# Kernel tuning notes

Measured on AMD Instinct MI355X. Metric: run time of the kernel, lower is better.

The kernel has to match this reference:

```python
import jax, jax.numpy as jnp
import numpy as np

P = 64      # num_proxies
S = 4096    # num_samples
D = 128     # embed_dim
H = 2       # nhead
HD = D // H # head dim


def _edge_index():
    # dense bipartite edges: (p -> s) and (s -> p) for every proxy/sample pair
    p = np.arange(P)
    s = np.arange(S) + P
    pp = np.repeat(p, S)
    ss = np.tile(s, P)
    src = np.concatenate([pp, ss])
    dst = np.concatenate([ss, pp])
    return jnp.asarray(np.stack([src, dst]), dtype=jnp.int32)  # [2, 2*P*S]


def setup_inputs() -> dict:
    key = jax.random.key(0)
    ks = jax.random.split(key, 13)
    lin = lambda k, o, i: jax.random.normal(k, (o, i), dtype=jnp.float32) * (1.0 / np.sqrt(i))
    return {
        "x": jax.random.normal(ks[0], (S, D), dtype=jnp.float32),
        "proxies": jax.random.normal(ks[1], (P, D), dtype=jnp.float32),
        "Wq": lin(ks[2], D, D), "bq": jnp.zeros((D,), jnp.float32),
        "Wk": lin(ks[3], D, D), "bk": jnp.zeros((D,), jnp.float32),
        "Wv": lin(ks[4], D, D), "bv": jnp.zeros((D,), jnp.float32),
        "Wo": lin(ks[5], D, D), "bo": jnp.zeros((D,), jnp.float32),
        "Wfc": lin(ks[6], D, D), "bfc": jnp.zeros((D,), jnp.float32),
        "edge_index": _edge_index(),
    }


def reference(x, proxies, Wq, bq, Wk, bk, Wv, bv, Wo, bo, Wfc, bfc, edge_index):
    feats = jnp.concatenate([proxies, x], axis=0)  # [N, D], N = P + S
    N = feats.shape[0]
    q = (feats @ Wq.T + bq).reshape(N, H, HD)
    k = (feats @ Wk.T + bk).reshape(N, H, HD)
    v = (feats @ Wv.T + bv).reshape(N, H, HD)
    src, dst = edge_index[0], edge_index[1]
    # per-edge attention logits [E, H]
    scores = jnp.einsum('ehd,ehd->eh', q[dst], k[src]) / jnp.sqrt(jnp.float32(HD))
    # scatter-softmax over incoming edges of each target node
    smax = jax.ops.segment_max(scores, dst, num_segments=N)
    ex = jnp.exp(scores - smax[dst])
    denom = jax.ops.segment_sum(ex, dst, num_segments=N)
    alpha = ex / denom[dst]                                   # [E, H]
    agg = jax.ops.segment_sum(alpha[:, :, None] * v[src], dst, num_segments=N)  # [N, H, HD]
    h = agg.reshape(N, D) @ Wo.T + bo
    h = jax.nn.relu(h)  # nn.Dropout in eval mode = identity
    preds = h @ Wfc.T + bfc
    return preds[P:], h[P:]
```

## Files before the change

### kernel.cpp

```cpp
#include <hip/hip_runtime.h>
#include <hip/hip_bf16.h>

#define SS 4096
#define DD 128
#define PP 64
#define NH 2
#define HDIM 64

typedef unsigned short u16;
typedef __attribute__((ext_vector_type(8))) short short8;
typedef __attribute__((ext_vector_type(4))) float float4v;

__device__ inline float bf2f(u16 u) {
    union { unsigned int i; float f; } v; v.i = ((unsigned int)u) << 16; return v.f;
}
__device__ inline u16 f2bf(float f) {
    union { float f; unsigned int i; } v; v.f = f;
    unsigned int i = v.i;
    return (u16)((i + 0x7fffu + ((i >> 16) & 1u)) >> 16);
}

__device__ inline bool detect_f32(const void* raw) {
    const u16* w = (const u16*)raw;
    const int lane = threadIdx.x & 63;
    bool hit = false;
    #pragma unroll
    for (int j = 0; j < 4; ++j) {
        u16 x = w[lane * 4 + j];
        int e = (x >> 7) & 0xFF;
        hit |= (e >= 0xBF);
    }
    return __ballot(hit) != 0ull;
}

template<bool F32>
__device__ inline float lds1(const void* p, int idx) {
    if constexpr (F32) return ((const float*)p)[idx];
    else               return bf2f(((const u16*)p)[idx]);
}

template<bool F32>
__device__ inline short8 ld8(const void* p, int idx) {
    if constexpr (!F32) {
        return *(const short8*)((const u16*)p + idx);
    } else {
        const float* f = (const float*)p + idx;
        float4 a = *(const float4*)f;
        float4 b = *(const float4*)(f + 4);
        short8 r;
        r[0] = (short)f2bf(a.x); r[1] = (short)f2bf(a.y);
        r[2] = (short)f2bf(a.z); r[3] = (short)f2bf(a.w);
        r[4] = (short)f2bf(b.x); r[5] = (short)f2bf(b.y);
        r[6] = (short)f2bf(b.z); r[7] = (short)f2bf(b.w);
        return r;
    }
}

template<bool F32>
__device__ inline void st1(void* p, size_t idx, float v) {
    if constexpr (F32) ((float*)p)[idx] = v;
    else               ((u16*)p)[idx]   = f2bf(v);
}

template<bool F32>
__device__ void fused_impl(
    const void* __restrict__ x,    const void* __restrict__ proxies,
    const void* __restrict__ Wq,  const void* __restrict__ bq,
    const void* __restrict__ Wk,  const void* __restrict__ bk,
    const void* __restrict__ Wv,  const void* __restrict__ bv,
    const void* __restrict__ Wo,  const void* __restrict__ bo,
    const void* __restrict__ Wfc, const void* __restrict__ bfc,
    void* __restrict__ d_out)
{
    __shared__ __attribute__((aligned(16))) u16   K_lds[PP][136];
    __shared__ __attribute__((aligned(16))) u16   VT_lds[DD][72];
    __shared__ __attribute__((aligned(16))) u16   q_lds[16][136];
    __shared__ __attribute__((aligned(16))) float sc_lds[NH][16][68];
    __shared__ __attribute__((aligned(16))) u16   al_lds[NH][16][72];
    __shared__ __attribute__((aligned(16))) u16   ag_lds[16][136];
    __shared__ __attribute__((aligned(16))) u16   h_lds[16][136];

    const int tid  = threadIdx.x;
    const int wave = tid >> 6;
    const int lane = tid & 63;
    const int lm   = lane & 15;
    const int quad = lane >> 4;
    const int s0   = blockIdx.x * 16;

    {
        float4v accK[4][2], accV[4][2];
        #pragma unroll
        for (int rt = 0; rt < 4; ++rt)
            #pragma unroll
            for (int ci = 0; ci < 2; ++ci) {
                accK[rt][ci] = (float4v){0,0,0,0};
                accV[rt][ci] = (float4v){0,0,0,0};
            }
        #pragma unroll
        for (int kt = 0; kt < 4; ++kt) {
            short8 a[4];
            #pragma unroll
            for (int rt = 0; rt < 4; ++rt)
                a[rt] = ld8<F32>(proxies, (rt * 16 + lm) * DD + kt * 32 + quad * 8);
            #pragma unroll
            for (int ci = 0; ci < 2; ++ci) {
                int d = (2 * wave + ci) * 16 + lm;
                short8 bK = ld8<F32>(Wk, d * DD + kt * 32 + quad * 8);
                short8 bV = ld8<F32>(Wv, d * DD + kt * 32 + quad * 8);
                #pragma unroll
                for (int rt = 0; rt < 4; ++rt) {
                    accK[rt][ci] = __builtin_amdgcn_mfma_f32_16x16x32_bf16(a[rt], bK, accK[rt][ci], 0, 0, 0);
                    accV[rt][ci] = __builtin_amdgcn_mfma_f32_16x16x32_bf16(a[rt], bV, accV[rt][ci], 0, 0, 0);
                }
            }
        }
        #pragma unroll
        for (int ci = 0; ci < 2; ++ci) {
            int d = (2 * wave + ci) * 16 + lm;
            float bkv = lds1<F32>(bk, d);
            float bvv = lds1<F32>(bv, d);
            #pragma unroll
            for (int rt = 0; rt < 4; ++rt)
                #pragma unroll
                for (int r = 0; r < 4; ++r) {
                    int p = rt * 16 + quad * 4 + r;
                    K_lds[p][d]  = f2bf(accK[rt][ci][r] + bkv);
                    VT_lds[d][p] = f2bf(accV[rt][ci][r] + bvv);
                }
        }
    }

    {
        float4v acc[2] = {{0,0,0,0},{0,0,0,0}};
        #pragma unroll
        for (int kt = 0; kt < 4; ++kt) {
            short8 a = ld8<F32>(x, (s0 + lm) * DD + kt * 32 + quad * 8);
            #pragma unroll
            for (int nt = 0; nt < 2; ++nt) {
                int d = (2 * wave + nt) * 16 + lm;
                short8 b = ld8<F32>(Wq, d * DD + kt * 32 + quad * 8);
                acc[nt] = __builtin_amdgcn_mfma_f32_16x16x32_bf16(a, b, acc[nt], 0, 0, 0);
            }
        }
        #pragma unroll
        for (int nt = 0; nt < 2; ++nt) {
            int col = (2 * wave + nt) * 16 + lm;
            float bias = lds1<F32>(bq, col);
            #pragma unroll
            for (int r = 0; r < 4; ++r)
                q_lds[quad * 4 + r][col] = f2bf(acc[nt][r] + bias);
        }
    }
    __syncthreads();

    const int head = wave >> 1;
    const int wh   = wave & 1;
    {
        float4v acc[2] = {{0,0,0,0},{0,0,0,0}};
        #pragma unroll
        for (int kt = 0; kt < 2; ++kt) {
            short8 a = *(const short8*)(&q_lds[lm][head * HDIM + kt * 32 + quad * 8]);
            #pragma unroll
            for (int nt = 0; nt < 2; ++nt) {
                int p = (wh * 2 + nt) * 16 + lm;
                short8 b = *(const short8*)(&K_lds[p][head * HDIM + kt * 32 + quad * 8]);
                acc[nt] = __builtin_amdgcn_mfma_f32_16x16x32_bf16(a, b, acc[nt], 0, 0, 0);
            }
        }
        const float scale = 0.125f;
        #pragma unroll
        for (int nt = 0; nt < 2; ++nt) {
            int p = (wh * 2 + nt) * 16 + lm;
            #pragma unroll
            for (int r = 0; r < 4; ++r)
                sc_lds[head][quad * 4 + r][p] = acc[nt][r] * scale;
        }
    }
    __syncthreads();

    if (tid < 64) {
        int s = tid & 15, hh = (tid >> 4) & 1, half = tid >> 5;
        const float* row = &sc_lds[hh][s][0];
        float m = -1e30f;
        #pragma unroll
        for (int j = 0; j < 32; ++j) m = fmaxf(m, row[half * 32 + j]);
        m = fmaxf(m, __shfl_xor(m, 32));
        float e[32], sum = 0.f;
        #pragma unroll
        for (int j = 0; j < 32; ++j) {
            e[j] = __expf(row[half * 32 + j] - m);
            sum += e[j];
        }
        sum += __shfl_xor(sum, 32);
        float inv = 1.f / sum;
        #pragma unroll
        for (int j = 0; j < 32; ++j)
            al_lds[hh][s][half * 32 + j] = f2bf(e[j] * inv);
    }
    __syncthreads();

    {
        float4v acc[2] = {{0,0,0,0},{0,0,0,0}};
        #pragma unroll
        for (int kt = 0; kt < 2; ++kt) {
            short8 a = *(const short8*)(&al_lds[head][lm][kt * 32 + quad * 8]);
            #pragma unroll
            for (int nt = 0; nt < 2; ++nt) {
                int hd = (wh * 2 + nt) * 16 + lm;
                short8 b = *(const short8*)(&VT_lds[head * HDIM + hd][kt * 32 + quad * 8]);
                acc[nt] = __builtin_amdgcn_mfma_f32_16x16x32_bf16(a, b, acc[nt], 0, 0, 0);
            }
        }
        #pragma unroll
        for (int nt = 0; nt < 2; ++nt) {
            int col = head * HDIM + (wh * 2 + nt) * 16 + lm;
            #pragma unroll
            for (int r = 0; r < 4; ++r)
                ag_lds[quad * 4 + r][col] = f2bf(acc[nt][r]);
        }
    }
    __syncthreads();

    {
        float4v acc[2] = {{0,0,0,0},{0,0,0,0}};
        #pragma unroll
        for (int kt = 0; kt < 4; ++kt) {
            short8 a = *(const short8*)(&ag_lds[lm][kt * 32 + quad * 8]);
            #pragma unroll
            for (int nt = 0; nt < 2; ++nt) {
                int d = (2 * wave + nt) * 16 + lm;
                short8 b = ld8<F32>(Wo, d * DD + kt * 32 + quad * 8);
                acc[nt] = __builtin_amdgcn_mfma_f32_16x16x32_bf16(a, b, acc[nt], 0, 0, 0);
            }
        }
        #pragma unroll
        for (int nt = 0; nt < 2; ++nt) {
            int col = (2 * wave + nt) * 16 + lm;
            float bias = lds1<F32>(bo, col);
            #pragma unroll
            for (int r = 0; r < 4; ++r) {
                int row = quad * 4 + r;
                float hv = fmaxf(acc[nt][r] + bias, 0.f);
                h_lds[row][col] = f2bf(hv);
                st1<F32>(d_out, (size_t)SS * DD + (size_t)(s0 + row) * DD + col, hv);
            }
        }
    }
    __syncthreads();

    {
        float4v acc[2] = {{0,0,0,0},{0,0,0,0}};
        #pragma unroll
        for (int kt = 0; kt < 4; ++kt) {
            short8 a = *(const short8*)(&h_lds[lm][kt * 32 + quad * 8]);
            #pragma unroll
            for (int nt = 0; nt < 2; ++nt) {
                int d = (2 * wave + nt) * 16 + lm;
                short8 b = ld8<F32>(Wfc, d * DD + kt * 32 + quad * 8);
                acc[nt] = __builtin_amdgcn_mfma_f32_16x16x32_bf16(a, b, acc[nt], 0, 0, 0);
            }
        }
        #pragma unroll
        for (int nt = 0; nt < 2; ++nt) {
            int col = (2 * wave + nt) * 16 + lm;
            float bias = lds1<F32>(bfc, col);
            #pragma unroll
            for (int r = 0; r < 4; ++r) {
                int row = quad * 4 + r;
                st1<F32>(d_out, (size_t)(s0 + row) * DD + col, acc[nt][r] + bias);
            }
        }
    }
}

__global__ __launch_bounds__(256) void fused_gnn(
    const void* x,   const void* proxies,
    const void* Wq,  const void* bq,
    const void* Wk,  const void* bk,
    const void* Wv,  const void* bv,
    const void* Wo,  const void* bo,
    const void* Wfc, const void* bfc,
    void* d_out)
{
    if (detect_f32(x))
        fused_impl<true >(x, proxies, Wq, bq, Wk, bk, Wv, bv, Wo, bo, Wfc, bfc, d_out);
    else
        fused_impl<false>(x, proxies, Wq, bq, Wk, bk, Wv, bv, Wo, bo, Wfc, bfc, d_out);
}

extern "C" void kernel_launch(void* const* d_in, const int* in_sizes, int n_in,
                              void* d_out, int out_size, void* d_ws, size_t ws_size,
                              hipStream_t stream) {
    fused_gnn<<<SS / 16, 256, 0, stream>>>(
        d_in[0], d_in[1], d_in[2], d_in[3], d_in[4], d_in[5], d_in[6],
        d_in[7], d_in[8], d_in[9], d_in[10], d_in[11], d_out);
}
```

Baseline: 96.13 us.

## Prefetch x, Wo, Wfc and biases at kernel start; parallelize softmax across all threads

Issues the global loads for the x tile, the Wo and Wfc weight fragments and the biases at kernel entry, so their latency overlaps the K/V proxy projection rather than sitting on the critical path of later stages. The softmax is also redistributed from 64 threads handling 32 elements each to all 256 threads handling 8 elements each, using shuffle reductions. The prefetch keeps 20 extra short8 fragments live across the whole kernel, which raises register pressure and may reduce occupancy or cause spills.

```diff
diff --git a/kernel.cpp b/kernel.cpp
--- a/kernel.cpp
+++ b/kernel.cpp
@@ -87,6 +87,28 @@
     const int quad = lane >> 4;
     const int s0   = blockIdx.x * 16;
 
+    short8 x_pf[4], wo_pf[2][4], wfc_pf[2][4];
+    #pragma unroll
+    for (int kt = 0; kt < 4; ++kt)
+        x_pf[kt] = ld8<F32>(x, (s0 + lm) * DD + kt * 32 + quad * 8);
+    #pragma unroll
+    for (int nt = 0; nt < 2; ++nt) {
+        int d = (2 * wave + nt) * 16 + lm;
+        #pragma unroll
+        for (int kt = 0; kt < 4; ++kt) {
+            wo_pf[nt][kt]  = ld8<F32>(Wo,  d * DD + kt * 32 + quad * 8);
+            wfc_pf[nt][kt] = ld8<F32>(Wfc, d * DD + kt * 32 + quad * 8);
+        }
+    }
+    float bo_v[2], bfc_v[2], bq_v[2];
+    #pragma unroll
+    for (int nt = 0; nt < 2; ++nt) {
+        int col = (2 * wave + nt) * 16 + lm;
+        bo_v[nt]  = lds1<F32>(bo,  col);
+        bfc_v[nt] = lds1<F32>(bfc, col);
+        bq_v[nt]  = lds1<F32>(bq,  col);
+    }
+
     {
         float4v accK[4][2], accV[4][2];
         #pragma unroll
@@ -134,21 +156,19 @@
         float4v acc[2] = {{0,0,0,0},{0,0,0,0}};
         #pragma unroll
         for (int kt = 0; kt < 4; ++kt) {
-            short8 a = ld8<F32>(x, (s0 + lm) * DD + kt * 32 + quad * 8);
             #pragma unroll
             for (int nt = 0; nt < 2; ++nt) {
                 int d = (2 * wave + nt) * 16 + lm;
                 short8 b = ld8<F32>(Wq, d * DD + kt * 32 + quad * 8);
-                acc[nt] = __builtin_amdgcn_mfma_f32_16x16x32_bf16(a, b, acc[nt], 0, 0, 0);
+                acc[nt] = __builtin_amdgcn_mfma_f32_16x16x32_bf16(x_pf[kt], b, acc[nt], 0, 0, 0);
             }
         }
         #pragma unroll
         for (int nt = 0; nt < 2; ++nt) {
             int col = (2 * wave + nt) * 16 + lm;
-            float bias = lds1<F32>(bq, col);
             #pragma unroll
             for (int r = 0; r < 4; ++r)
-                q_lds[quad * 4 + r][col] = f2bf(acc[nt][r] + bias);
+                q_lds[quad * 4 + r][col] = f2bf(acc[nt][r] + bq_v[nt]);
         }
     }
     __syncthreads();
@@ -178,24 +198,27 @@
     }
     __syncthreads();
 
-    if (tid < 64) {
-        int s = tid & 15, hh = (tid >> 4) & 1, half = tid >> 5;
-        const float* row = &sc_lds[hh][s][0];
-        float m = -1e30f;
-        #pragma unroll
-        for (int j = 0; j < 32; ++j) m = fmaxf(m, row[half * 32 + j]);
-        m = fmaxf(m, __shfl_xor(m, 32));
-        float e[32], sum = 0.f;
-        #pragma unroll
-        for (int j = 0; j < 32; ++j) {
-            e[j] = __expf(row[half * 32 + j] - m);
-            sum += e[j];
-        }
-        sum += __shfl_xor(sum, 32);
+    {
+        int r  = tid >> 3;
+        int g  = tid & 7;
+        int s  = r & 15, hh = r >> 4;
+        const float* row = &sc_lds[hh][s][g * 8];
+        float v[8], m = -1e30f;
+        #pragma unroll
+        for (int j = 0; j < 8; ++j) { v[j] = row[j]; m = fmaxf(m, v[j]); }
+        m = fmaxf(m, __shfl_xor(m, 1));
+        m = fmaxf(m, __shfl_xor(m, 2));
+        m = fmaxf(m, __shfl_xor(m, 4));
+        float sum = 0.f;
+        #pragma unroll
+        for (int j = 0; j < 8; ++j) { v[j] = __expf(v[j] - m); sum += v[j]; }
+        sum += __shfl_xor(sum, 1);
+        sum += __shfl_xor(sum, 2);
+        sum += __shfl_xor(sum, 4);
         float inv = 1.f / sum;
         #pragma unroll
-        for (int j = 0; j < 32; ++j)
-            al_lds[hh][s][half * 32 + j] = f2bf(e[j] * inv);
+        for (int j = 0; j < 8; ++j)
+            al_lds[hh][s][g * 8 + j] = f2bf(v[j] * inv);
     }
     __syncthreads();
 
@@ -227,20 +250,16 @@
         for (int kt = 0; kt < 4; ++kt) {
             short8 a = *(const short8*)(&ag_lds[lm][kt * 32 + quad * 8]);
             #pragma unroll
-            for (int nt = 0; nt < 2; ++nt) {
-                int d = (2 * wave + nt) * 16 + lm;
-                short8 b = ld8<F32>(Wo, d * DD + kt * 32 + quad * 8);
-                acc[nt] = __builtin_amdgcn_mfma_f32_16x16x32_bf16(a, b, acc[nt], 0, 0, 0);
-            }
+            for (int nt = 0; nt < 2; ++nt)
+                acc[nt] = __builtin_amdgcn_mfma_f32_16x16x32_bf16(a, wo_pf[nt][kt], acc[nt], 0, 0, 0);
         }
         #pragma unroll
         for (int nt = 0; nt < 2; ++nt) {
             int col = (2 * wave + nt) * 16 + lm;
-            float bias = lds1<F32>(bo, col);
             #pragma unroll
             for (int r = 0; r < 4; ++r) {
                 int row = quad * 4 + r;
-                float hv = fmaxf(acc[nt][r] + bias, 0.f);
+                float hv = fmaxf(acc[nt][r] + bo_v[nt], 0.f);
                 h_lds[row][col] = f2bf(hv);
                 st1<F32>(d_out, (size_t)SS * DD + (size_t)(s0 + row) * DD + col, hv);
             }
@@ -254,20 +273,16 @@
         for (int kt = 0; kt < 4; ++kt) {
             short8 a = *(const short8*)(&h_lds[lm][kt * 32 + quad * 8]);
             #pragma unroll
-            for (int nt = 0; nt < 2; ++nt) {
-                int d = (2 * wave + nt) * 16 + lm;
-                short8 b = ld8<F32>(Wfc, d * DD + kt * 32 + quad * 8);
-                acc[nt] = __builtin_amdgcn_mfma_f32_16x16x32_bf16(a, b, acc[nt], 0, 0, 0);
-            }
+            for (int nt = 0; nt < 2; ++nt)
+                acc[nt] = __builtin_amdgcn_mfma_f32_16x16x32_bf16(a, wfc_pf[nt][kt], acc[nt], 0, 0, 0);
         }
         #pragma unroll
         for (int nt = 0; nt < 2; ++nt) {
             int col = (2 * wave + nt) * 16 + lm;
-            float bias = lds1<F32>(bfc, col);
             #pragma unroll
             for (int r = 0; r < 4; ++r) {
                 int row = quad * 4 + r;
-                st1<F32>(d_out, (size_t)(s0 + row) * DD + col, acc[nt][r] + bias);
+                st1<F32>(d_out, (size_t)(s0 + row) * DD + col, acc[nt][r] + bfc_v[nt]);
             }
         }
     }
```

Result: no change. 96.66 us (+0.5%).
